# Kernel tuning notes

Measured on AMD Instinct MI355X. Metric: run time of the kernel, lower is better.

Reference implementation:

```python
import jax, jax.numpy as jnp
import numpy as np

EPS = 1e-6      # vn_layers EPS
BN_EPS = 1e-5   # torch BatchNorm eps
NEG = 0.2       # LeakyReLU negative slope
K = 20


def setup_inputs() -> dict:
    key = jax.random.key(0)
    ks = jax.random.split(key, 10)
    B, C, N = 4, 384, 2048
    return {
        'x': jax.random.normal(ks[0], (B, C, N), jnp.float32),
        'w_kc1_feat': jax.random.normal(ks[1], (21, 256), jnp.float32) * 0.05,
        'w_kc1_dir': jax.random.normal(ks[2], (21, 256), jnp.float32) * 0.05,
        'w_kc2_feat': jax.random.normal(ks[3], (21, 21), jnp.float32) * 0.05,
        'w_kc2_dir': jax.random.normal(ks[4], (21, 21), jnp.float32) * 0.05,
        'w_pool_dir': jax.random.normal(ks[5], (21, 21), jnp.float32) * 0.05,
        'w_conv1': jax.random.normal(ks[6], (256, 63), jnp.float32) * 0.05,
        'w_conv2': jax.random.normal(ks[7], (128, 256), jnp.float32) * 0.05,
        'w_conv3': jax.random.normal(ks[8], (1, 128), jnp.float32) * 0.05,
        'b_conv3': jnp.zeros((1,), jnp.float32),
    }


def knn_idx(xf, k):
    # xf: (B, C, N) -> (B, N, k) indices of k nearest neighbors (neg sq dist top-k)
    inner = -2.0 * jnp.einsum('bcn,bcm->bnm', xf, xf)
    xx = jnp.sum(xf * xf, axis=1)  # (B, N)
    neg_dist = -(xx[:, :, None] + inner + xx[:, None, :])
    _, idx = jax.lax.top_k(neg_dist, k)
    return idx


def get_graph_feature(x, k):
    # x: (B, C3, 3, N) -> (B, 2*C3, 3, N, k)
    B, C3, _, N = x.shape
    xf = x.reshape(B, C3 * 3, N)
    idx = knn_idx(xf, k)                      # (B, N, k)
    xt = jnp.transpose(xf, (0, 2, 1))         # (B, N, C3*3)
    feat = jax.vmap(lambda a, i: a[i])(xt, idx)  # (B, N, k, C3*3)
    feat = feat.reshape(B, N, k, C3, 3)
    xc = xt.reshape(B, N, 1, C3, 3)
    out = jnp.concatenate([feat - xc, jnp.broadcast_to(xc, feat.shape)], axis=3)
    return jnp.transpose(out, (0, 3, 4, 1, 2))  # (B, 2C3, 3, N, k)


def vn_bn(x):
    # VNBatchNorm (dim=5), training-mode batch stats, no affine (gamma=1, beta=0)
    norm = jnp.linalg.norm(x, axis=2) + EPS          # (B, C, N, K)
    mean = jnp.mean(norm, axis=(0, 2, 3), keepdims=True)
    var = jnp.mean((norm - mean) ** 2, axis=(0, 2, 3), keepdims=True)
    norm_bn = (norm - mean) / jnp.sqrt(var + BN_EPS)
    return x / norm[:, :, None] * norm_bn[:, :, None]


def vn_block(x, w_feat, w_dir):
    # VNLinearLeakyReLU: x (B, Cin, 3, N, K)
    p = jnp.einsum('oc,bcvnk->bovnk', w_feat, x)
    p = vn_bn(p)
    d = jnp.einsum('oc,bcvnk->bovnk', w_dir, x)
    dot = jnp.sum(p * d, axis=2, keepdims=True)
    d2 = jnp.sum(d * d, axis=2, keepdims=True)
    proj = p - (dot / (d2 + EPS)) * d
    return NEG * p + (1.0 - NEG) * jnp.where(dot >= 0, p, proj)


def vn_max_pool(x, w_dir):
    # x: (B, C, 3, N, K) -> (B, C, 3, N)
    d = jnp.einsum('oc,bcvnk->bovnk', w_dir, x)
    dot = jnp.sum(x * d, axis=2, keepdims=True)        # (B, C, 1, N, K)
    idx = jnp.argmax(dot, axis=-1)                     # (B, C, 1, N)
    idx = jnp.broadcast_to(idx[..., None], x.shape[:-1] + (1,))
    return jnp.take_along_axis(x, idx, axis=-1)[..., 0]


def conv_bn_lrelu(x, w):
    # 1x1 Conv1d (no bias) + BatchNorm1d (batch stats) + LeakyReLU(0.2)
    y = jnp.einsum('oc,bcn->bon', w, x)
    mean = jnp.mean(y, axis=(0, 2), keepdims=True)
    var = jnp.mean((y - mean) ** 2, axis=(0, 2), keepdims=True)
    y = (y - mean) / jnp.sqrt(var + BN_EPS)
    return jnp.where(y >= 0, y, NEG * y)


def reference(x, w_kc1_feat, w_kc1_dir, w_kc2_feat, w_kc2_dir, w_pool_dir,
              w_conv1, w_conv2, w_conv3, b_conv3):
    B, C, N = x.shape
    h = x[:, None]                      # (B, 1, in_dim, N) -> treated as (B, C3, 3, N)
    h = h.reshape(B, C // 3, 3, N)
    h = get_graph_feature(h, K)         # (B, 2*C//3, 3, N, K)
    h = vn_block(h, w_kc1_feat, w_kc1_dir)
    h = vn_block(h, w_kc2_feat, w_kc2_dir)
    h = vn_max_pool(h, w_pool_dir)      # (B, 21, 3, N)
    h = h.reshape(B, 63, N)
    h = conv_bn_lrelu(h, w_conv1)
    h = conv_bn_lrelu(h, w_conv2)
    # dropout is identity (inference); final 1x1 conv with bias
    out = jnp.einsum('oc,bcn->bon', w_conv3, h) + b_conv3[None, :, None]
    return out[:, 0, :]                 # squeeze(dim=-2) -> (B, N)
```

## Files before the change

### kernel.cpp

```cpp
#include <hip/hip_runtime.h>
#include <cstddef>

#define BB 4
#define CC 384
#define NPT 2048
#define KNN 20
#define NCAND 32
#define NCH 21
#define NKT (NPT*KNN)
#define TOT (BB*NKT)
#define EPSD 1e-6
#define BNEPSD 1e-5
#define EPSF 1e-6f
#define BNEPS 1e-5f
#define NEGS 0.2f

__global__ __launch_bounds__(256) void k_zero(float* p, int n) {
    int t = blockIdx.x*256 + threadIdx.x;
    if (t < n) p[t] = 0.f;
}

__global__ __launch_bounds__(256) void k_xt(const float* __restrict__ x, float* __restrict__ xT) {
    __shared__ float tile[64][65];
    int n0 = blockIdx.x*64, c0 = blockIdx.y*64, b = blockIdx.z;
    int tx = threadIdx.x & 63, ty = threadIdx.x >> 6;
    const float* xb = x + (size_t)b*CC*NPT;
    #pragma unroll
    for (int r = 0; r < 64; r += 4)
        tile[r+ty][tx] = xb[(size_t)(c0+r+ty)*NPT + n0 + tx];
    __syncthreads();
    float* xtb = xT + (size_t)b*NPT*CC;
    #pragma unroll
    for (int r = 0; r < 64; r += 4)
        xtb[(size_t)(n0+r+ty)*CC + c0 + tx] = tile[tx][r+ty];
}

__global__ __launch_bounds__(256) void k_xx(const float* __restrict__ xT, float* __restrict__ xx,
                                            double* __restrict__ xxd) {
    int pid = blockIdx.x*4 + (threadIdx.x >> 6);
    int lane = threadIdx.x & 63;
    const float* row = xT + (size_t)pid*CC;
    double acc = 0.0;
    #pragma unroll
    for (int c = lane; c < CC; c += 64) { double v = (double)row[c]; acc += v*v; }
    #pragma unroll
    for (int st = 32; st > 0; st >>= 1) acc += __shfl_down(acc, st);
    if (lane == 0) { xx[pid] = (float)acc; xxd[pid] = acc; }
}

__global__ __launch_bounds__(256) void k_gram(const float* __restrict__ x, const float* __restrict__ xx,
                                              float* __restrict__ scores4) {
    __shared__ float As[16][64];
    __shared__ float Bs[16][64];
    int tid = blockIdx.x;
    int b = blockIdx.y;
    int by = 0, rem = tid;
    while (rem >= 32 - by) { rem -= 32 - by; by++; }
    int bx = by + rem;
    int n0 = by*64, m0 = bx*64;
    int t = threadIdx.x;
    int tx = t & 15, ty = t >> 4;
    const float* xb = x + (size_t)b*CC*NPT;
    float* scores = scores4 + (size_t)b*NPT*NPT;
    float acc[4][4] = {};
    for (int c0 = 0; c0 < CC; c0 += 16) {
        #pragma unroll
        for (int i = 0; i < 4; i++) {
            int e = t + i*256;
            int cc = e >> 6, col = e & 63;
            As[cc][col] = xb[(size_t)(c0+cc)*NPT + n0 + col];
            Bs[cc][col] = xb[(size_t)(c0+cc)*NPT + m0 + col];
        }
        __syncthreads();
        #pragma unroll
        for (int kk = 0; kk < 16; kk++) {
            float4 a  = *(const float4*)&As[kk][ty*4];
            float4 bv = *(const float4*)&Bs[kk][tx*4];
            acc[0][0] += a.x*bv.x; acc[0][1] += a.x*bv.y; acc[0][2] += a.x*bv.z; acc[0][3] += a.x*bv.w;
            acc[1][0] += a.y*bv.x; acc[1][1] += a.y*bv.y; acc[1][2] += a.y*bv.z; acc[1][3] += a.y*bv.w;
            acc[2][0] += a.z*bv.x; acc[2][1] += a.z*bv.y; acc[2][2] += a.z*bv.z; acc[2][3] += a.z*bv.w;
            acc[3][0] += a.w*bv.x; acc[3][1] += a.w*bv.y; acc[3][2] += a.w*bv.z; acc[3][3] += a.w*bv.w;
        }
        __syncthreads();
    }
    int nb = n0 + ty*4, mb = m0 + tx*4;
    float xn[4], xm[4];
    #pragma unroll
    for (int i = 0; i < 4; i++) { xn[i] = xx[b*NPT + nb + i]; xm[i] = xx[b*NPT + mb + i]; }
    float val[4][4];
    #pragma unroll
    for (int i = 0; i < 4; i++)
        #pragma unroll
        for (int j = 0; j < 4; j++) {
            val[i][j] = 2.f*acc[i][j] - xn[i] - xm[j];
            scores[(size_t)(nb+i)*NPT + mb + j] = val[i][j];
        }
    if (bx != by) {
        #pragma unroll
        for (int j = 0; j < 4; j++)
            #pragma unroll
            for (int i = 0; i < 4; i++)
                scores[(size_t)(mb+j)*NPT + nb + i] = val[i][j];
    }
}

__global__ __launch_bounds__(256) void k_topk(const float* __restrict__ scores4, int* __restrict__ candout) {
    int n = blockIdx.x, b = blockIdx.y;
    const float* row = scores4 + ((size_t)b*NPT + n)*NPT;
    unsigned key[8];
    #pragma unroll
    for (int w = 0; w < 8; w++) {
        unsigned u = __float_as_uint(row[threadIdx.x + w*256]);
        key[w] = (u & 0x80000000u) ? ~u : (u | 0x80000000u);
    }
    __shared__ int hist[4][257];
    __shared__ int histsum[256];
    __shared__ unsigned s_pfx;
    __shared__ int s_need, s_slot, s_tie;
    __shared__ unsigned long long tiel[256];
    int wv = threadIdx.x >> 6;
    if (threadIdx.x == 0) { s_pfx = 0u; s_need = NCAND; s_slot = 0; s_tie = 0; }
    #pragma unroll
    for (int pass = 0; pass < 3; pass++) {
        int sh = (pass == 0) ? 24 : (pass == 1 ? 16 : 8);
        unsigned maskhi = (pass == 0) ? 0u : (pass == 1 ? 0xFF000000u : 0xFFFF0000u);
        hist[0][threadIdx.x] = 0; hist[1][threadIdx.x] = 0;
        hist[2][threadIdx.x] = 0; hist[3][threadIdx.x] = 0;
        __syncthreads();
        unsigned pfx = s_pfx;
        #pragma unroll
        for (int w = 0; w < 8; w++) {
            unsigned v = key[w];
            if ((v & maskhi) == (pfx & maskhi))
                atomicAdd(&hist[wv][(v >> sh) & 0xFF], 1);
        }
        __syncthreads();
        histsum[threadIdx.x] = hist[0][threadIdx.x] + hist[1][threadIdx.x]
                             + hist[2][threadIdx.x] + hist[3][threadIdx.x];
        __syncthreads();
        if (threadIdx.x < 64) {
            int l = threadIdx.x, base = l*4;
            int c0 = histsum[base], c1 = histsum[base+1], c2 = histsum[base+2], c3 = histsum[base+3];
            int mysum = c0 + c1 + c2 + c3;
            int suf = mysum;
            #pragma unroll
            for (int st = 1; st < 64; st <<= 1) {
                int u2 = __shfl_down(suf, st);
                if (l + st >= 64) u2 = 0;
                suf += u2;
            }
            int need = s_need;
            int sufNext = suf - mysum;
            if (suf >= need && sufNext < need) {
                int s3 = sufNext + c3, s2p = s3 + c2, s1p = s2p + c1;
                int B, Sb1;
                if (s3 >= need)       { B = base+3; Sb1 = sufNext; }
                else if (s2p >= need) { B = base+2; Sb1 = s3; }
                else if (s1p >= need) { B = base+1; Sb1 = s2p; }
                else                  { B = base;   Sb1 = s1p; }
                s_pfx = s_pfx | ((unsigned)B << sh);
                s_need = need - Sb1;
            }
        }
        __syncthreads();
    }
    unsigned pfx24 = s_pfx & 0xFFFFFF00u;
    int* outp = candout + ((size_t)b*NPT + n)*NCAND;
    #pragma unroll
    for (int w = 0; w < 8; w++) {
        unsigned v = key[w];
        unsigned hi = v & 0xFFFFFF00u;
        int i = threadIdx.x + w*256;
        if (hi > pfx24) {
            int s = atomicAdd(&s_slot, 1);
            outp[s] = i;
        } else if (hi == pfx24) {
            int ti = atomicAdd(&s_tie, 1);
            if (ti < 256) tiel[ti] = ((unsigned long long)v << 32) | (unsigned)(NPT-1-i);
        }
    }
    __syncthreads();
    if (threadIdx.x == 0) {
        int A = s_slot, r = s_need, T = s_tie < 256 ? s_tie : 256;
        for (int kk = 0; kk < r; kk++) {
            unsigned long long best = 0ull; int bj = 0;
            for (int j2 = 0; j2 < T; j2++) if (tiel[j2] > best) { best = tiel[j2]; bj = j2; }
            tiel[bj] = 0ull;
            outp[A + kk] = NPT-1-(int)(best & 0xFFFFFFFFu);
        }
    }
}

__global__ __launch_bounds__(256) void k_rescore(const float* __restrict__ xT, const double* __restrict__ xxd,
                                                 const int* __restrict__ cand, int* __restrict__ idxout) {
    __shared__ float xn[CC];
    __shared__ double sc[NCAND];
    __shared__ int ci[NCAND];
    int t = blockIdx.x;
    int b = t >> 11;
    const float* xrow = xT + (size_t)t*CC;
    for (int i = threadIdx.x; i < CC; i += 256) xn[i] = xrow[i];
    if (threadIdx.x < NCAND) ci[threadIdx.x] = cand[(size_t)t*NCAND + threadIdx.x];
    __syncthreads();
    int j = threadIdx.x >> 3, l = threadIdx.x & 7;
    int m = ci[j];
    const float* xm = xT + ((size_t)b*NPT + m)*CC;
    double acc = 0.0;
    int cbase = l*48;
    #pragma unroll 8
    for (int c = 0; c < 48; c++) acc += (double)xn[cbase+c] * (double)xm[cbase+c];
    acc += __shfl_down(acc, 4, 8);
    acc += __shfl_down(acc, 2, 8);
    acc += __shfl_down(acc, 1, 8);
    if (l == 0) sc[j] = 2.0*acc - xxd[t] - xxd[(size_t)b*NPT + m];
    __syncthreads();
    if (threadIdx.x < 64) {
        double v = (threadIdx.x < NCAND) ? sc[threadIdx.x] : -1e300;
        int oi = (threadIdx.x < NCAND) ? ci[threadIdx.x] : NPT;
        for (int kk = 0; kk < KNN; kk++) {
            double bv = v; int bo = oi;
            #pragma unroll
            for (int st = 16; st > 0; st >>= 1) {
                double ov = __shfl_xor(bv, st, 32);
                int    oo = __shfl_xor(bo, st, 32);
                if (ov > bv || (ov == bv && oo < bo)) { bv = ov; bo = oo; }
            }
            if (threadIdx.x == 0) idxout[(size_t)t*KNN + kk] = bo;
            if (oi == bo) v = -1e300;
        }
    }
}

__global__ __launch_bounds__(256) void k_pq_d(const float* __restrict__ xT,
                                              const float* __restrict__ wf, const float* __restrict__ wd,
                                              double* __restrict__ Pf, double* __restrict__ Qf,
                                              double* __restrict__ Pd, double* __restrict__ Qd) {
    __shared__ float xs[4][CC];
    __shared__ float wfa[128*NCH];
    __shared__ float wfb[128*NCH];
    __shared__ float wda[128*NCH];
    __shared__ float wdb[128*NCH];
    int pt = threadIdx.x >> 6;
    int ov = threadIdx.x & 63;
    int row0 = blockIdx.x*4;
    for (int i = threadIdx.x; i < 4*CC; i += 256)
        xs[i/CC][i%CC] = xT[(size_t)(row0 + i/CC)*CC + (i%CC)];
    for (int i = threadIdx.x; i < 128*NCH; i += 256) {
        int o2 = i >> 7, c3 = i & 127;
        wfa[c3*NCH+o2] = wf[o2*256 + c3];
        wfb[c3*NCH+o2] = wf[o2*256 + 128 + c3];
        wda[c3*NCH+o2] = wd[o2*256 + c3];
        wdb[c3*NCH+o2] = wd[o2*256 + 128 + c3];
    }
    __syncthreads();
    if (ov >= 63) return;
    int o = ov / 3, v = ov % 3;
    const float* xp = &xs[pt][v];
    double pf = 0.0, qf = 0.0, pd = 0.0, qd = 0.0;
    #pragma unroll 4
    for (int c3 = 0; c3 < 128; c3++) {
        double xv = (double)xp[c3*3];
        double waf = (double)wfa[c3*NCH+o], wbf = (double)wfb[c3*NCH+o];
        double wad = (double)wda[c3*NCH+o], wbd = (double)wdb[c3*NCH+o];
        pf += waf*xv; qf += (wbf-waf)*xv;
        pd += wad*xv; qd += (wbd-wad)*xv;
    }
    size_t off = (size_t)(row0 + pt)*64 + ov;
    Pf[off] = pf; Qf[off] = qf; Pd[off] = pd; Qd[off] = qd;
}

__global__ __launch_bounds__(256) void k_bn1_part(const double* __restrict__ Pf, const double* __restrict__ Qf,
                                                  const int* __restrict__ idx, double* __restrict__ part) {
    __shared__ double red[4][42];
    int t = blockIdx.x*256 + threadIdx.x;
    int bn = t / KNN;
    int n = bn & (NPT-1); int b = bn >> 11;
    int m = idx[t];
    const double* PF = Pf + ((size_t)b*NPT + m)*64;
    const double* QF = Qf + ((size_t)b*NPT + n)*64;
    int wave = threadIdx.x >> 6;
    #pragma unroll
    for (int o = 0; o < NCH; o++) {
        double p0 = PF[o*3+0] + QF[o*3+0];
        double p1 = PF[o*3+1] + QF[o*3+1];
        double p2 = PF[o*3+2] + QF[o*3+2];
        double nr = sqrt(p0*p0 + p1*p1 + p2*p2) + EPSD;
        double a = nr, c2 = nr*nr;
        #pragma unroll
        for (int st = 32; st > 0; st >>= 1) { a += __shfl_down(a, st); c2 += __shfl_down(c2, st); }
        if ((threadIdx.x & 63) == 0) { red[wave][o] = a; red[wave][NCH+o] = c2; }
    }
    __syncthreads();
    if (threadIdx.x < 42)
        part[(size_t)blockIdx.x*42 + threadIdx.x] =
            red[0][threadIdx.x] + red[1][threadIdx.x] + red[2][threadIdx.x] + red[3][threadIdx.x];
}

__global__ __launch_bounds__(256) void k_fin_d(const double* __restrict__ part, double* __restrict__ st,
                                               int nblk, double cnt) {
    __shared__ double r0[4], r1[4];
    int o = blockIdx.x;
    double s0 = 0.0, s1 = 0.0;
    for (int i = threadIdx.x; i < nblk; i += 256) {
        s0 += part[(size_t)i*42 + o];
        s1 += part[(size_t)i*42 + NCH + o];
    }
    #pragma unroll
    for (int stp = 32; stp > 0; stp >>= 1) { s0 += __shfl_down(s0, stp); s1 += __shfl_down(s1, stp); }
    int wv = threadIdx.x >> 6;
    if ((threadIdx.x & 63) == 0) { r0[wv] = s0; r1[wv] = s1; }
    __syncthreads();
    if (threadIdx.x == 0) {
        double sum = r0[0]+r0[1]+r0[2]+r0[3];
        double ssq = r1[0]+r1[1]+r1[2]+r1[3];
        double mean = sum / cnt;
        double var = ssq / cnt - mean*mean;
        if (var < 0.0) var = 0.0;
        st[o] = mean;
        st[NCH+o] = 1.0 / sqrt(var + BNEPSD);
    }
}

__global__ __launch_bounds__(256) void k_b1_bn2part(const double* __restrict__ Pf, const double* __restrict__ Qf,
                                                    const double* __restrict__ Pd, const double* __restrict__ Qd,
                                                    const int* __restrict__ idx, const double* __restrict__ st1,
                                                    const float* __restrict__ w2f_g, double* __restrict__ part) {
    __shared__ double h1L[32][65];
    __shared__ double w2s[NCH*NCH];
    __shared__ double s1[42];
    __shared__ double wred[4][42];
    int tid = threadIdx.x;
    int p = tid >> 3, j = tid & 7;
    int t = blockIdx.x*32 + p;
    for (int i = tid; i < NCH*NCH; i += 256) w2s[i] = (double)w2f_g[i];
    if (tid < 42) s1[tid] = st1[tid];
    int bn = t / KNN;
    int n = bn & (NPT-1), b = bn >> 11;
    int m = idx[t];
    const double* PF = Pf + ((size_t)b*NPT + m)*64;
    const double* QF = Qf + ((size_t)b*NPT + n)*64;
    const double* PD = Pd + ((size_t)b*NPT + m)*64;
    const double* QD = Qd + ((size_t)b*NPT + n)*64;
    __syncthreads();
    for (int o = j; o < NCH; o += 8) {
        double p0 = PF[o*3+0] + QF[o*3+0];
        double p1 = PF[o*3+1] + QF[o*3+1];
        double p2 = PF[o*3+2] + QF[o*3+2];
        double d0 = PD[o*3+0] + QD[o*3+0];
        double d1 = PD[o*3+1] + QD[o*3+1];
        double d2 = PD[o*3+2] + QD[o*3+2];
        double nr = sqrt(p0*p0 + p1*p1 + p2*p2) + EPSD;
        double fac = (nr - s1[o]) * s1[NCH+o] / nr;
        p0 *= fac; p1 *= fac; p2 *= fac;
        double dot = p0*d0 + p1*d1 + p2*d2;
        double dd  = d0*d0 + d1*d1 + d2*d2;
        double coef = dot / (dd + EPSD);
        double w0 = (dot >= 0.0) ? p0 : (p0 - coef*d0);
        double w1 = (dot >= 0.0) ? p1 : (p1 - coef*d1);
        double w2 = (dot >= 0.0) ? p2 : (p2 - coef*d2);
        h1L[p][o*3+0] = 0.2*p0 + 0.8*w0;
        h1L[p][o*3+1] = 0.2*p1 + 0.8*w1;
        h1L[p][o*3+2] = 0.2*p2 + 0.8*w2;
    }
    __syncthreads();
    double s[3] = {0.0,0.0,0.0}, q[3] = {0.0,0.0,0.0};
    {
        int oi = 0;
        for (int o = j; o < NCH; o += 8, oi++) {
            double a0 = 0.0, a1 = 0.0, a2 = 0.0;
            #pragma unroll
            for (int c = 0; c < NCH; c++) {
                double w = w2s[o*NCH+c];
                a0 += w*h1L[p][c*3+0]; a1 += w*h1L[p][c*3+1]; a2 += w*h1L[p][c*3+2];
            }
            double nr = sqrt(a0*a0 + a1*a1 + a2*a2) + EPSD;
            s[oi] = nr; q[oi] = nr*nr;
        }
    }
    #pragma unroll
    for (int st = 8; st < 64; st <<= 1) {
        #pragma unroll
        for (int u = 0; u < 3; u++) { s[u] += __shfl_down(s[u], st); q[u] += __shfl_down(q[u], st); }
    }
    if ((tid & 63) < 8) {
        int wv = tid >> 6, oi = 0;
        for (int o = j; o < NCH; o += 8, oi++) { wred[wv][o] = s[oi]; wred[wv][NCH+o] = q[oi]; }
    }
    __syncthreads();
    if (tid < 42)
        part[(size_t)blockIdx.x*42 + tid] = wred[0][tid]+wred[1][tid]+wred[2][tid]+wred[3][tid];
}

__global__ __launch_bounds__(256) void k_apply_d(const double* __restrict__ Pf, const double* __restrict__ Qf,
                                                 const double* __restrict__ Pd, const double* __restrict__ Qd,
                                                 const int* __restrict__ idx,
                                                 const double* __restrict__ st1, const double* __restrict__ st2,
                                                 const float* __restrict__ w2f_g, const float* __restrict__ w2d_g,
                                                 const float* __restrict__ wp_g,
                                                 float* __restrict__ h2f, double* __restrict__ dots) {
    __shared__ double hL[32][65];
    __shared__ double w2fs[NCH*NCH];
    __shared__ double w2ds[NCH*NCH];
    __shared__ double wps[NCH*NCH];
    __shared__ double s1[42], s2[42];
    int tid = threadIdx.x;
    int p = tid >> 3, j = tid & 7;
    int t = blockIdx.x*32 + p;
    for (int i = tid; i < NCH*NCH; i += 256) {
        w2fs[i] = (double)w2f_g[i]; w2ds[i] = (double)w2d_g[i]; wps[i] = (double)wp_g[i];
    }
    if (tid < 42) { s1[tid] = st1[tid]; s2[tid] = st2[tid]; }
    int k = t % KNN; int bn = t / KNN;
    int n = bn & (NPT-1), b = bn >> 11;
    int m = idx[t];
    const double* PF = Pf + ((size_t)b*NPT + m)*64;
    const double* QF = Qf + ((size_t)b*NPT + n)*64;
    const double* PD = Pd + ((size_t)b*NPT + m)*64;
    const double* QD = Qd + ((size_t)b*NPT + n)*64;
    __syncthreads();
    #pragma unroll
    for (int oi = 0; oi < 3; oi++) {
        int o = j + oi*8;
        if (o < NCH) {
            double p0 = PF[o*3+0] + QF[o*3+0];
            double p1 = PF[o*3+1] + QF[o*3+1];
            double p2 = PF[o*3+2] + QF[o*3+2];
            double d0 = PD[o*3+0] + QD[o*3+0];
            double d1 = PD[o*3+1] + QD[o*3+1];
            double d2 = PD[o*3+2] + QD[o*3+2];
            double nr = sqrt(p0*p0 + p1*p1 + p2*p2) + EPSD;
            double fac = (nr - s1[o]) * s1[NCH+o] / nr;
            p0 *= fac; p1 *= fac; p2 *= fac;
            double dot = p0*d0 + p1*d1 + p2*d2;
            double dd  = d0*d0 + d1*d1 + d2*d2;
            double coef = dot / (dd + EPSD);
            double w0 = (dot >= 0.0) ? p0 : (p0 - coef*d0);
            double w1 = (dot >= 0.0) ? p1 : (p1 - coef*d1);
            double w2 = (dot >= 0.0) ? p2 : (p2 - coef*d2);
            hL[p][o*3+0] = 0.2*p0 + 0.8*w0;
            hL[p][o*3+1] = 0.2*p1 + 0.8*w1;
            hL[p][o*3+2] = 0.2*p2 + 0.8*w2;
        }
    }
    __syncthreads();
    double h2r[3][3];
    #pragma unroll
    for (int oi = 0; oi < 3; oi++) {
        int o = j + oi*8;
        if (o < NCH) {
            double p0 = 0.0, p1 = 0.0, p2 = 0.0, d0 = 0.0, d1 = 0.0, d2 = 0.0;
            #pragma unroll
            for (int c = 0; c < NCH; c++) {
                double wa = w2fs[o*NCH+c], wb = w2ds[o*NCH+c];
                double x0 = hL[p][c*3+0], x1 = hL[p][c*3+1], x2 = hL[p][c*3+2];
                p0 += wa*x0; p1 += wa*x1; p2 += wa*x2;
                d0 += wb*x0; d1 += wb*x1; d2 += wb*x2;
            }
            double nr = sqrt(p0*p0 + p1*p1 + p2*p2) + EPSD;
            double fac = (nr - s2[o]) * s2[NCH+o] / nr;
            p0 *= fac; p1 *= fac; p2 *= fac;
            double dot = p0*d0 + p1*d1 + p2*d2;
            double dd  = d0*d0 + d1*d1 + d2*d2;
            double coef = dot / (dd + EPSD);
            double w0 = (dot >= 0.0) ? p0 : (p0 - coef*d0);
            double w1 = (dot >= 0.0) ? p1 : (p1 - coef*d1);
            double w2 = (dot >= 0.0) ? p2 : (p2 - coef*d2);
            double h0 = 0.2*p0 + 0.8*w0, h1v = 0.2*p1 + 0.8*w1, h2v = 0.2*p2 + 0.8*w2;
            h2r[oi][0] = h0; h2r[oi][1] = h1v; h2r[oi][2] = h2v;
            h2f[((size_t)(b*63 + o*3+0)*NPT + n)*KNN + k] = (float)h0;
            h2f[((size_t)(b*63 + o*3+1)*NPT + n)*KNN + k] = (float)h1v;
            h2f[((size_t)(b*63 + o*3+2)*NPT + n)*KNN + k] = (float)h2v;
        }
    }
    __syncthreads();
    #pragma unroll
    for (int oi = 0; oi < 3; oi++) {
        int o = j + oi*8;
        if (o < NCH) {
            hL[p][o*3+0] = h2r[oi][0];
            hL[p][o*3+1] = h2r[oi][1];
            hL[p][o*3+2] = h2r[oi][2];
        }
    }
    __syncthreads();
    #pragma unroll
    for (int oi = 0; oi < 3; oi++) {
        int o = j + oi*8;
        if (o < NCH) {
            double dv0 = 0.0, dv1 = 0.0, dv2 = 0.0;
            #pragma unroll
            for (int c = 0; c < NCH; c++) {
                double w = wps[o*NCH+c];
                dv0 += w*hL[p][c*3+0]; dv1 += w*hL[p][c*3+1]; dv2 += w*hL[p][c*3+2];
            }
            double dt = hL[p][o*3+0]*dv0 + hL[p][o*3+1]*dv1 + hL[p][o*3+2]*dv2;
            dots[(((size_t)b*NCH + o)*NPT + n)*KNN + k] = dt;
        }
    }
}

__global__ __launch_bounds__(32) void k_pool_d(const double* __restrict__ dots, const float* __restrict__ h2f,
                                               float* __restrict__ pooled) {
    int b = blockIdx.x >> 11, n = blockIdx.x & (NPT-1);
    int o = threadIdx.x;
    if (o >= NCH) return;
    const double* dp = dots + (((size_t)b*NCH + o)*NPT + n)*KNN;
    double best = dp[0]; int bk = 0;
    #pragma unroll
    for (int k = 1; k < KNN; k++) { double v = dp[k]; if (v > best) { best = v; bk = k; } }
    #pragma unroll
    for (int v = 0; v < 3; v++)
        pooled[((size_t)b*63 + o*3+v)*NPT + n] = h2f[(((size_t)b*63 + o*3+v)*NPT + n)*KNN + bk];
}

__global__ __launch_bounds__(256) void k_conv1(const float* __restrict__ pooled, const float* __restrict__ w1,
                                               float* __restrict__ y1, float* __restrict__ sums) {
    int n = blockIdx.x*256 + threadIdx.x;
    int o = blockIdx.y, b = blockIdx.z;
    const float* pb = pooled + (size_t)b*63*NPT + n;
    const float* wo = w1 + o*63;
    float acc = 0.f;
    #pragma unroll
    for (int c = 0; c < 63; c++) acc += wo[c]*pb[(size_t)c*NPT];
    y1[((size_t)b*256 + o)*NPT + n] = acc;
    float a = acc, c2 = acc*acc;
    #pragma unroll
    for (int st = 32; st > 0; st >>= 1) { a += __shfl_down(a, st); c2 += __shfl_down(c2, st); }
    __shared__ float ra[4], rc[4];
    int wv = threadIdx.x >> 6;
    if ((threadIdx.x & 63) == 0) { ra[wv] = a; rc[wv] = c2; }
    __syncthreads();
    if (threadIdx.x == 0) {
        atomicAdd(&sums[o], ra[0]+ra[1]+ra[2]+ra[3]);
        atomicAdd(&sums[256+o], rc[0]+rc[1]+rc[2]+rc[3]);
    }
}

__global__ void k_finalize(const float* __restrict__ sums, float* __restrict__ stats, float invcnt, int nch) {
    int o = blockIdx.x*blockDim.x + threadIdx.x;
    if (o >= nch) return;
    float mean = sums[o]*invcnt;
    float var = sums[nch+o]*invcnt - mean*mean;
    if (var < 0.f) var = 0.f;
    stats[o] = mean;
    stats[nch+o] = 1.0f / sqrtf(var + BNEPS);
}

__global__ __launch_bounds__(256) void k_act(float* __restrict__ y, const float* __restrict__ stats, int nch) {
    int t = blockIdx.x*256 + threadIdx.x;
    int o = (t >> 11) % nch;
    float z = (y[t] - stats[o]) * stats[nch+o];
    y[t] = z >= 0.f ? z : NEGS*z;
}

__global__ __launch_bounds__(256) void k_conv2(const float* __restrict__ z1, const float* __restrict__ w2,
                                               float* __restrict__ y2, float* __restrict__ sums) {
    int n = blockIdx.x*256 + threadIdx.x;
    int o = blockIdx.y, b = blockIdx.z;
    const float* pb = z1 + (size_t)b*256*NPT + n;
    const float* wo = w2 + o*256;
    float acc = 0.f;
    #pragma unroll 4
    for (int c = 0; c < 256; c++) acc += wo[c]*pb[(size_t)c*NPT];
    y2[((size_t)b*128 + o)*NPT + n] = acc;
    float a = acc, c2 = acc*acc;
    #pragma unroll
    for (int st = 32; st > 0; st >>= 1) { a += __shfl_down(a, st); c2 += __shfl_down(c2, st); }
    __shared__ float ra[4], rc[4];
    int wv = threadIdx.x >> 6;
    if ((threadIdx.x & 63) == 0) { ra[wv] = a; rc[wv] = c2; }
    __syncthreads();
    if (threadIdx.x == 0) {
        atomicAdd(&sums[o], ra[0]+ra[1]+ra[2]+ra[3]);
        atomicAdd(&sums[128+o], rc[0]+rc[1]+rc[2]+rc[3]);
    }
}

__global__ __launch_bounds__(256) void k_final(const float* __restrict__ y2, const float* __restrict__ w3,
                                               const float* __restrict__ b3, const float* __restrict__ stats,
                                               float* __restrict__ out) {
    int t = blockIdx.x*256 + threadIdx.x;
    int n = t & (NPT-1); int b = t >> 11;
    const float* yb = y2 + (size_t)b*128*NPT + n;
    float acc = b3[0];
    #pragma unroll 4
    for (int c = 0; c < 128; c++) {
        float z = (yb[(size_t)c*NPT] - stats[c]) * stats[128+c];
        z = z >= 0.f ? z : NEGS*z;
        acc += w3[c]*z;
    }
    out[t] = acc;
}

extern "C" void kernel_launch(void* const* d_in, const int* in_sizes, int n_in,
                              void* d_out, int out_size, void* d_ws, size_t ws_size,
                              hipStream_t stream) {
    const float* x   = (const float*)d_in[0];
    const float* w1f = (const float*)d_in[1];
    const float* w1d = (const float*)d_in[2];
    const float* w2f = (const float*)d_in[3];
    const float* w2d = (const float*)d_in[4];
    const float* wp  = (const float*)d_in[5];
    const float* wc1 = (const float*)d_in[6];
    const float* wc2 = (const float*)d_in[7];
    const float* wc3 = (const float*)d_in[8];
    const float* bc3 = (const float*)d_in[9];
    float* out = (float*)d_out;

    float* ws = (float*)d_ws;
    float*  scores4 = ws;
    float*  xxf     = ws + 16777216;
    double* xxd     = (double*)(ws + 16785408);
    int*    cand    = (int*)(ws + 16801792);
    int*    idx     = (int*)(ws + 17063936);
    float*  xT      = ws + 17227776;
    double* Pfd     = (double*)(ws + 20373504);
    double* Qfd     = (double*)(ws + 21422080);
    double* Pdd     = (double*)(ws + 22470656);
    double* Qdd     = (double*)(ws + 23519232);
    double* part1   = (double*)(ws + 24567808);
    double* part2   = (double*)(ws + 24621568);
    double* st1     = (double*)(ws + 25051648);
    double* st2     = (double*)(ws + 25051776);
    float*  sums_f  = ws + 25051904;
    float*  stats_f = ws + 25052928;
    double* dots    = (double*)(ws + 25053952);
    float*  h2f     = ws + 31935232;
    float*  pooled  = ws + 42257152;
    float*  y1      = ws + 42773248;
    float*  y2      = ws + 44870400;

    k_zero<<<4, 256, 0, stream>>>(sums_f, 1024);
    k_xt<<<dim3(NPT/64, CC/64, BB), 256, 0, stream>>>(x, xT);
    k_xx<<<BB*NPT/4, 256, 0, stream>>>(xT, xxf, xxd);
    k_gram<<<dim3(528, BB), 256, 0, stream>>>(x, xxf, scores4);
    k_topk<<<dim3(NPT, BB), 256, 0, stream>>>(scores4, cand);
    k_rescore<<<BB*NPT, 256, 0, stream>>>(xT, xxd, cand, idx);
    k_pq_d<<<BB*NPT/4, 256, 0, stream>>>(xT, w1f, w1d, Pfd, Qfd, Pdd, Qdd);
    k_bn1_part<<<TOT/256, 256, 0, stream>>>(Pfd, Qfd, idx, part1);
    k_fin_d<<<NCH, 256, 0, stream>>>(part1, st1, TOT/256, (double)TOT);
    k_b1_bn2part<<<TOT/32, 256, 0, stream>>>(Pfd, Qfd, Pdd, Qdd, idx, st1, w2f, part2);
    k_fin_d<<<NCH, 256, 0, stream>>>(part2, st2, TOT/32, (double)TOT);
    k_apply_d<<<TOT/32, 256, 0, stream>>>(Pfd, Qfd, Pdd, Qdd, idx, st1, st2, w2f, w2d, wp, h2f, dots);
    k_pool_d<<<BB*NPT, 32, 0, stream>>>(dots, h2f, pooled);
    k_conv1<<<dim3(NPT/256, 256, BB), 256, 0, stream>>>(pooled, wc1, y1, sums_f);
    k_finalize<<<1, 256, 0, stream>>>(sums_f, stats_f, 1.f/(float)(BB*NPT), 256);
    k_act<<<BB*256*NPT/256, 256, 0, stream>>>(y1, stats_f, 256);
    k_conv2<<<dim3(NPT/256, 128, BB), 256, 0, stream>>>(y1, wc2, y2, sums_f+512);
    k_finalize<<<1, 128, 0, stream>>>(sums_f+512, stats_f+512, 1.f/(float)(BB*NPT), 128);
    k_final<<<BB*NPT/256, 256, 0, stream>>>(y2, wc3, bc3, stats_f+512, out);
}
```

Before: 629.4 us.

## Fuse VN apply and max-pool into one per-point kernel

Merges the apply kernel with the pooling kernel so that each block handles one point with all 20 neighbours. The per-neighbour dot products and features now stay in shared memory, and the max-pool is done in-block. This removes the large global writes and reads of h2f and dots and one kernel launch. In exchange, 256-thread blocks use only 240 threads (12 per neighbour), the grid has fewer but heavier blocks, and the weights are reloaded into shared memory per point instead of per 32 neighbour slots.

```diff
diff --git a/kernel.cpp b/kernel.cpp
--- a/kernel.cpp
+++ b/kernel.cpp
@@ -391,37 +391,42 @@
         part[(size_t)blockIdx.x*42 + tid] = wred[0][tid]+wred[1][tid]+wred[2][tid]+wred[3][tid];
 }
 
-__global__ __launch_bounds__(256) void k_apply_d(const double* __restrict__ Pf, const double* __restrict__ Qf,
-                                                 const double* __restrict__ Pd, const double* __restrict__ Qd,
-                                                 const int* __restrict__ idx,
-                                                 const double* __restrict__ st1, const double* __restrict__ st2,
-                                                 const float* __restrict__ w2f_g, const float* __restrict__ w2d_g,
-                                                 const float* __restrict__ wp_g,
-                                                 float* __restrict__ h2f, double* __restrict__ dots) {
-    __shared__ double hL[32][65];
+__global__ __launch_bounds__(256) void k_apply_pool(const double* __restrict__ Pf, const double* __restrict__ Qf,
+                                                    const double* __restrict__ Pd, const double* __restrict__ Qd,
+                                                    const int* __restrict__ idx,
+                                                    const double* __restrict__ st1, const double* __restrict__ st2,
+                                                    const float* __restrict__ w2f_g, const float* __restrict__ w2d_g,
+                                                    const float* __restrict__ wp_g,
+                                                    float* __restrict__ pooled) {
+    __shared__ double hL[KNN][65];
     __shared__ double w2fs[NCH*NCH];
     __shared__ double w2ds[NCH*NCH];
     __shared__ double wps[NCH*NCH];
     __shared__ double s1[42], s2[42];
+    __shared__ double dotsL[NCH][KNN+1];
+    __shared__ int midx[KNN];
     int tid = threadIdx.x;
-    int p = tid >> 3, j = tid & 7;
-    int t = blockIdx.x*32 + p;
+    int bn = blockIdx.x;
+    int n = bn & (NPT-1), b = bn >> 11;
     for (int i = tid; i < NCH*NCH; i += 256) {
         w2fs[i] = (double)w2f_g[i]; w2ds[i] = (double)w2d_g[i]; wps[i] = (double)wp_g[i];
     }
     if (tid < 42) { s1[tid] = st1[tid]; s2[tid] = st2[tid]; }
-    int k = t % KNN; int bn = t / KNN;
-    int n = bn & (NPT-1), b = bn >> 11;
-    int m = idx[t];
-    const double* PF = Pf + ((size_t)b*NPT + m)*64;
-    const double* QF = Qf + ((size_t)b*NPT + n)*64;
-    const double* PD = Pd + ((size_t)b*NPT + m)*64;
-    const double* QD = Qd + ((size_t)b*NPT + n)*64;
-    __syncthreads();
-    #pragma unroll
-    for (int oi = 0; oi < 3; oi++) {
-        int o = j + oi*8;
-        if (o < NCH) {
+    if (tid < KNN) midx[tid] = idx[(size_t)bn*KNN + tid];
+    __syncthreads();
+    int p = tid / 12, j = tid % 12;
+    bool act = (p < KNN);
+    const double* QF = Qf + (size_t)bn*64;
+    const double* QD = Qd + (size_t)bn*64;
+    const double* PF = Pf;
+    const double* PD = Pd;
+    if (act) {
+        int m = midx[p];
+        PF = Pf + ((size_t)b*NPT + m)*64;
+        PD = Pd + ((size_t)b*NPT + m)*64;
+    }
+    if (act) {
+        for (int o = j; o < NCH; o += 12) {
             double p0 = PF[o*3+0] + QF[o*3+0];
             double p1 = PF[o*3+1] + QF[o*3+1];
             double p2 = PF[o*3+2] + QF[o*3+2];
@@ -443,11 +448,11 @@
         }
     }
     __syncthreads();
-    double h2r[3][3];
-    #pragma unroll
-    for (int oi = 0; oi < 3; oi++) {
-        int o = j + oi*8;
-        if (o < NCH) {
+    double h2a0=0, h2a1=0, h2a2=0, h2b0=0, h2b1=0, h2b2=0;
+    int oA = j, oB = j + 12;
+    if (act) {
+        {
+            int o = oA;
             double p0 = 0.0, p1 = 0.0, p2 = 0.0, d0 = 0.0, d1 = 0.0, d2 = 0.0;
             #pragma unroll
             for (int c = 0; c < NCH; c++) {
@@ -465,52 +470,57 @@
             double w0 = (dot >= 0.0) ? p0 : (p0 - coef*d0);
             double w1 = (dot >= 0.0) ? p1 : (p1 - coef*d1);
             double w2 = (dot >= 0.0) ? p2 : (p2 - coef*d2);
-            double h0 = 0.2*p0 + 0.8*w0, h1v = 0.2*p1 + 0.8*w1, h2v = 0.2*p2 + 0.8*w2;
-            h2r[oi][0] = h0; h2r[oi][1] = h1v; h2r[oi][2] = h2v;
-            h2f[((size_t)(b*63 + o*3+0)*NPT + n)*KNN + k] = (float)h0;
-            h2f[((size_t)(b*63 + o*3+1)*NPT + n)*KNN + k] = (float)h1v;
-            h2f[((size_t)(b*63 + o*3+2)*NPT + n)*KNN + k] = (float)h2v;
-        }
-    }
-    __syncthreads();
-    #pragma unroll
-    for (int oi = 0; oi < 3; oi++) {
-        int o = j + oi*8;
-        if (o < NCH) {
-            hL[p][o*3+0] = h2r[oi][0];
-            hL[p][o*3+1] = h2r[oi][1];
-            hL[p][o*3+2] = h2r[oi][2];
-        }
-    }
-    __syncthreads();
-    #pragma unroll
-    for (int oi = 0; oi < 3; oi++) {
-        int o = j + oi*8;
-        if (o < NCH) {
+            h2a0 = 0.2*p0 + 0.8*w0; h2a1 = 0.2*p1 + 0.8*w1; h2a2 = 0.2*p2 + 0.8*w2;
+        }
+        if (oB < NCH) {
+            int o = oB;
+            double p0 = 0.0, p1 = 0.0, p2 = 0.0, d0 = 0.0, d1 = 0.0, d2 = 0.0;
+            #pragma unroll
+            for (int c = 0; c < NCH; c++) {
+                double wa = w2fs[o*NCH+c], wb = w2ds[o*NCH+c];
+                double x0 = hL[p][c*3+0], x1 = hL[p][c*3+1], x2 = hL[p][c*3+2];
+                p0 += wa*x0; p1 += wa*x1; p2 += wa*x2;
+                d0 += wb*x0; d1 += wb*x1; d2 += wb*x2;
+            }
+            double nr = sqrt(p0*p0 + p1*p1 + p2*p2) + EPSD;
+            double fac = (nr - s2[o]) * s2[NCH+o] / nr;
+            p0 *= fac; p1 *= fac; p2 *= fac;
+            double dot = p0*d0 + p1*d1 + p2*d2;
+            double dd  = d0*d0 + d1*d1 + d2*d2;
+            double coef = dot / (dd + EPSD);
+            double w0 = (dot >= 0.0) ? p0 : (p0 - coef*d0);
+            double w1 = (dot >= 0.0) ? p1 : (p1 - coef*d1);
+            double w2 = (dot >= 0.0) ? p2 : (p2 - coef*d2);
+            h2b0 = 0.2*p0 + 0.8*w0; h2b1 = 0.2*p1 + 0.8*w1; h2b2 = 0.2*p2 + 0.8*w2;
+        }
+    }
+    __syncthreads();
+    if (act) {
+        hL[p][oA*3+0] = h2a0; hL[p][oA*3+1] = h2a1; hL[p][oA*3+2] = h2a2;
+        if (oB < NCH) { hL[p][oB*3+0] = h2b0; hL[p][oB*3+1] = h2b1; hL[p][oB*3+2] = h2b2; }
+    }
+    __syncthreads();
+    if (act) {
+        for (int o = j; o < NCH; o += 12) {
             double dv0 = 0.0, dv1 = 0.0, dv2 = 0.0;
             #pragma unroll
             for (int c = 0; c < NCH; c++) {
                 double w = wps[o*NCH+c];
                 dv0 += w*hL[p][c*3+0]; dv1 += w*hL[p][c*3+1]; dv2 += w*hL[p][c*3+2];
             }
-            double dt = hL[p][o*3+0]*dv0 + hL[p][o*3+1]*dv1 + hL[p][o*3+2]*dv2;
-            dots[(((size_t)b*NCH + o)*NPT + n)*KNN + k] = dt;
-        }
-    }
-}
-
-__global__ __launch_bounds__(32) void k_pool_d(const double* __restrict__ dots, const float* __restrict__ h2f,
-                                               float* __restrict__ pooled) {
-    int b = blockIdx.x >> 11, n = blockIdx.x & (NPT-1);
-    int o = threadIdx.x;
-    if (o >= NCH) return;
-    const double* dp = dots + (((size_t)b*NCH + o)*NPT + n)*KNN;
-    double best = dp[0]; int bk = 0;
-    #pragma unroll
-    for (int k = 1; k < KNN; k++) { double v = dp[k]; if (v > best) { best = v; bk = k; } }
-    #pragma unroll
-    for (int v = 0; v < 3; v++)
-        pooled[((size_t)b*63 + o*3+v)*NPT + n] = h2f[(((size_t)b*63 + o*3+v)*NPT + n)*KNN + bk];
+            dotsL[o][p] = hL[p][o*3+0]*dv0 + hL[p][o*3+1]*dv1 + hL[p][o*3+2]*dv2;
+        }
+    }
+    __syncthreads();
+    if (tid < NCH) {
+        int o = tid;
+        double best = dotsL[o][0]; int bk = 0;
+        #pragma unroll
+        for (int kk = 1; kk < KNN; kk++) { double v = dotsL[o][kk]; if (v > best) { best = v; bk = kk; } }
+        #pragma unroll
+        for (int u = 0; u < 3; u++)
+            pooled[((size_t)b*63 + o*3+u)*NPT + n] = (float)hL[bk][o*3+u];
+    }
 }
 
 __global__ __launch_bounds__(256) void k_conv1(const float* __restrict__ pooled, const float* __restrict__ w1,
@@ -624,11 +634,9 @@
     double* st2     = (double*)(ws + 25051776);
     float*  sums_f  = ws + 25051904;
     float*  stats_f = ws + 25052928;
-    double* dots    = (double*)(ws + 25053952);
-    float*  h2f     = ws + 31935232;
-    float*  pooled  = ws + 42257152;
-    float*  y1      = ws + 42773248;
-    float*  y2      = ws + 44870400;
+    float*  pooled  = ws + 25053952;
+    float*  y1      = ws + 25570048;
+    float*  y2      = ws + 27667200;
 
     k_zero<<<4, 256, 0, stream>>>(sums_f, 1024);
     k_xt<<<dim3(NPT/64, CC/64, BB), 256, 0, stream>>>(x, xT);
@@ -641,8 +649,7 @@
     k_fin_d<<<NCH, 256, 0, stream>>>(part1, st1, TOT/256, (double)TOT);
     k_b1_bn2part<<<TOT/32, 256, 0, stream>>>(Pfd, Qfd, Pdd, Qdd, idx, st1, w2f, part2);
     k_fin_d<<<NCH, 256, 0, stream>>>(part2, st2, TOT/32, (double)TOT);
-    k_apply_d<<<TOT/32, 256, 0, stream>>>(Pfd, Qfd, Pdd, Qdd, idx, st1, st2, w2f, w2d, wp, h2f, dots);
-    k_pool_d<<<BB*NPT, 32, 0, stream>>>(dots, h2f, pooled);
+    k_apply_pool<<<BB*NPT, 256, 0, stream>>>(Pfd, Qfd, Pdd, Qdd, idx, st1, st2, w2f, w2d, wp, pooled);
     k_conv1<<<dim3(NPT/256, 256, BB), 256, 0, stream>>>(pooled, wc1, y1, sums_f);
     k_finalize<<<1, 256, 0, stream>>>(sums_f, stats_f, 1.f/(float)(BB*NPT), 256);
     k_act<<<BB*256*NPT/256, 256, 0, stream>>>(y1, stats_f, 256);
```

After: 604.4 us (median of 2 runs). 4.0% less time.
